# Performance work log

Hardware: AMD Instinct MI355X
Metric: run time of the kernel (lower is better)

The kernel has to match this reference:

```python
import jax, jax.numpy as jnp
import numpy as np

NUM_USER = 100000
NUM_ITEM = 50000
N = NUM_USER + NUM_ITEM          # total nodes
D = 64                            # dim_latent
E = 2400000                       # nnz of sparse graph
NUM_LAYER = 3


def setup_inputs() -> dict:
    key = jax.random.key(0)
    k1, k2, k3, k4, k5 = jax.random.split(key, 5)
    user_emb = jax.random.normal(k1, (NUM_USER, D), dtype=jnp.float32)
    item_emb = jax.random.normal(k2, (NUM_ITEM, D), dtype=jnp.float32)
    graph_rows = jax.random.randint(k3, (E,), 0, N, dtype=jnp.int32)
    graph_cols = jax.random.randint(k4, (E,), 0, N, dtype=jnp.int32)
    # normalized-adjacency-like small positive values
    graph_vals = jax.random.uniform(k5, (E,), dtype=jnp.float32) * 0.01
    return {
        "user_emb": user_emb,
        "item_emb": item_emb,
        "graph_vals": graph_vals,
        "graph_rows": graph_rows,
        "graph_cols": graph_cols,
    }


def _spmm(vals, rows, cols, x):
    # sparse [N,N] @ dense [N,D] via gather + segment_sum
    gathered = vals[:, None] * x[cols]            # [E, D]
    return jax.ops.segment_sum(gathered, rows, num_segments=N)  # [N, D]


def reference(user_emb, item_emb, graph_vals, graph_rows, graph_cols):
    all_emb = jnp.concatenate([user_emb, item_emb], axis=0)   # [N, D]
    acc = all_emb
    emb = all_emb
    for _ in range(NUM_LAYER):
        emb = _spmm(graph_vals, graph_rows, graph_cols, emb)
        acc = acc + emb
    light_out = acc / jnp.float32(NUM_LAYER + 1)              # mean over layer dim
    return (light_out, user_emb, item_emb)
```

## Files before the change

kernel.cpp:

```cpp
#include <hip/hip_runtime.h>


#define NUM_USER 100000
#define NUM_ITEM 50000
#define NTOT     150000
#define DIM      64
#define NEDGE    2400000
#define ND       (NTOT * DIM)

#define RPB    256
#define NB     586
#define CAP    4736
#define CHUNK  4096
#define NCHUNK 586
#define EPT    16

static __device__ __forceinline__ unsigned short f2bf(float f) {
    unsigned u = __float_as_uint(f);
    u += 0x7FFFu + ((u >> 16) & 1u);
    return (unsigned short)(u >> 16);
}
static __device__ __forceinline__ float bf2f(unsigned short h) {
    return __uint_as_float(((unsigned)h) << 16);
}

__global__ __launch_bounds__(256) void initcur_kernel(int* __restrict__ cursor) {
    const int i = blockIdx.x * blockDim.x + threadIdx.x;
    if (i < NB) cursor[i] = i * CAP;
}

__global__ __launch_bounds__(256) void phaseA_kernel(
    const int*   __restrict__ rows,
    const int*   __restrict__ cols,
    const float* __restrict__ vals,
    int*            __restrict__ cursor,
    unsigned*       __restrict__ crG,
    unsigned short* __restrict__ vbG)
{
    __shared__ unsigned       s_cr[CHUNK];
    __shared__ unsigned short s_vb[CHUNK];
    __shared__ unsigned short s_bk[CHUNK];
    __shared__ int s_hist[NB];
    __shared__ int s_scan[NB];
    __shared__ int s_dst[NB];
    __shared__ int s_cur[NB];
    __shared__ int s_part[256];

    const int t    = threadIdx.x;
    const int base = blockIdx.x * CHUNK;
    const int n    = min(CHUNK, NEDGE - base);

    for (int i = t; i < NB; i += 256) s_hist[i] = 0;
    __syncthreads();

    int            mrow[EPT];
    unsigned       mcol[EPT];
    unsigned short mvb[EPT];
#pragma unroll
    for (int k = 0; k < EPT; ++k) {
        const int i = t + k * 256;
        if (i < n) {
            const int e = base + i;
            mrow[k] = rows[e];
            mcol[k] = (unsigned)cols[e];
            mvb[k]  = f2bf(vals[e]);
            atomicAdd(&s_hist[mrow[k] >> 8], 1);
        } else mrow[k] = -1;
    }
    __syncthreads();

    int loc[3]; int ssum = 0;
#pragma unroll
    for (int k = 0; k < 3; ++k) {
        const int i = t * 3 + k;
        loc[k] = (i < NB) ? s_hist[i] : 0;
        ssum += loc[k];
    }
    s_part[t] = ssum;
    __syncthreads();
    for (int o = 1; o < 256; o <<= 1) {
        const int v = (t >= o) ? s_part[t - o] : 0;
        __syncthreads();
        s_part[t] += v;
        __syncthreads();
    }
    int run = s_part[t] - ssum;
#pragma unroll
    for (int k = 0; k < 3; ++k) {
        const int i = t * 3 + k;
        if (i < NB) { s_scan[i] = run; run += loc[k]; }
    }
    __syncthreads();

    for (int i = t; i < NB; i += 256) {
        const int c = s_hist[i];
        s_dst[i] = c ? atomicAdd(&cursor[i], c) : 0;
        s_cur[i] = s_scan[i];
    }
    __syncthreads();

#pragma unroll
    for (int k = 0; k < EPT; ++k) {
        if (mrow[k] >= 0) {
            const int b   = mrow[k] >> 8;
            const int pos = atomicAdd(&s_cur[b], 1);
            s_cr[pos] = mcol[k] | ((unsigned)(mrow[k] & 255) << 18);
            s_vb[pos] = mvb[k];
            s_bk[pos] = (unsigned short)b;
        }
    }
    __syncthreads();

    for (int p = t; p < n; p += 256) {
        const int b = s_bk[p];
        const int g = s_dst[b] + (p - s_scan[b]);
        crG[g] = s_cr[p];
        vbG[g] = s_vb[p];
    }
}

__global__ __launch_bounds__(256) void phaseB_kernel(
    const int*      __restrict__ cursor,
    unsigned*       __restrict__ crG,
    unsigned short* __restrict__ vbG,
    int*            __restrict__ rowbeg,
    int*            __restrict__ rowend)
{
    __shared__ unsigned       s_cr[CAP];
    __shared__ unsigned short s_vb[CAP];
    __shared__ unsigned short s_idx[CAP];
    __shared__ int s_hist[RPB];
    __shared__ int s_scan[RPB];
    __shared__ int s_cur[RPB];

    const int b = blockIdx.x, t = threadIdx.x;
    const int gbase = b * CAP;
    const int cnt = cursor[b] - gbase;

    s_hist[t] = 0;
    __syncthreads();
    for (int p = t; p < cnt; p += 256) {
        const unsigned cr = crG[gbase + p];
        s_cr[p] = cr;
        s_vb[p] = vbG[gbase + p];
        atomicAdd(&s_hist[cr >> 18], 1);
    }
    __syncthreads();

    const int h = s_hist[t];
    s_scan[t] = h;
    __syncthreads();
    for (int o = 1; o < 256; o <<= 1) {
        const int v = (t >= o) ? s_scan[t - o] : 0;
        __syncthreads();
        s_scan[t] += v;
        __syncthreads();
    }
    const int excl = s_scan[t] - h;
    s_cur[t] = excl;
    __syncthreads();

    for (int p = t; p < cnt; p += 256) {
        const int r   = s_cr[p] >> 18;
        const int pos = atomicAdd(&s_cur[r], 1);
        s_idx[pos] = (unsigned short)p;
    }
    __syncthreads();

    for (int p = t; p < cnt; p += 256) {
        const int i = s_idx[p];
        crG[gbase + p] = s_cr[i];
        vbG[gbase + p] = s_vb[i];
    }
    const int row = b * RPB + t;
    if (row < NTOT) {
        rowbeg[row] = gbase + excl;
        rowend[row] = gbase + excl + h;
    }
}

__global__ __launch_bounds__(256) void convert_kernel(
    const float* __restrict__ user,
    const float* __restrict__ item,
    unsigned short* __restrict__ xb)
{
    const int nvec  = ND / 4;
    const int userv = NUM_USER * DIM / 4;
    for (int i = blockIdx.x * blockDim.x + threadIdx.x; i < nvec;
         i += gridDim.x * blockDim.x) {
        const float4 v = (i < userv) ? ((const float4*)user)[i]
                                     : ((const float4*)item)[i - userv];
        ushort4 o;
        o.x = f2bf(v.x); o.y = f2bf(v.y); o.z = f2bf(v.z); o.w = f2bf(v.w);
        ((ushort4*)xb)[i] = o;
    }
}

template<int MODE>
__global__ __launch_bounds__(256) void spmm_pull(
    const int*            __restrict__ rowbeg,
    const int*            __restrict__ rowend,
    const unsigned*       __restrict__ crG,
    const unsigned short* __restrict__ vbG,
    const unsigned short* __restrict__ xb,
    unsigned short*       __restrict__ destb,
    float*                __restrict__ acc,
    const float*          __restrict__ user,
    const float*          __restrict__ item,
    float*                __restrict__ out)
{
    const int r    = (blockIdx.x * 256 + threadIdx.x) >> 6;
    const int lane = threadIdx.x & 63;
    const int g    = lane >> 4;
    const int l    = lane & 15;

    const int beg = __builtin_amdgcn_readfirstlane(rowbeg[r]);
    const int end = __builtin_amdgcn_readfirstlane(rowend[r]);

    float r0 = 0.f, r1 = 0.f, r2 = 0.f, r3 = 0.f;
    for (int k = beg + g; k < end; k += 8) {
        const bool h1 = (k + 4) < end;
        const int  k1 = h1 ? k + 4 : k;
        const unsigned c0 = crG[k]  & 0x3FFFFu;
        const unsigned c1 = crG[k1] & 0x3FFFFu;
        const float    v0 = bf2f(vbG[k]);
        const float    v1 = h1 ? bf2f(vbG[k1]) : 0.f;
        const uint2 xa = *reinterpret_cast<const uint2*>(
                             xb + ((size_t)c0 << 6) + (l << 2));
        const uint2 xc = *reinterpret_cast<const uint2*>(
                             xb + ((size_t)c1 << 6) + (l << 2));
        r0 += v0 * bf2f((unsigned short)(xa.x & 0xFFFFu))
            + v1 * bf2f((unsigned short)(xc.x & 0xFFFFu));
        r1 += v0 * bf2f((unsigned short)(xa.x >> 16))
            + v1 * bf2f((unsigned short)(xc.x >> 16));
        r2 += v0 * bf2f((unsigned short)(xa.y & 0xFFFFu))
            + v1 * bf2f((unsigned short)(xc.y & 0xFFFFu));
        r3 += v0 * bf2f((unsigned short)(xa.y >> 16))
            + v1 * bf2f((unsigned short)(xc.y >> 16));
    }
    r0 += __shfl_xor(r0, 16); r0 += __shfl_xor(r0, 32);
    r1 += __shfl_xor(r1, 16); r1 += __shfl_xor(r1, 32);
    r2 += __shfl_xor(r2, 16); r2 += __shfl_xor(r2, 32);
    r3 += __shfl_xor(r3, 16); r3 += __shfl_xor(r3, 32);

    if (g == 0) {
        const int o = r * DIM + (l << 2);
        if (MODE == 0) {
            *reinterpret_cast<float4*>(acc + o) = make_float4(r0, r1, r2, r3);
        } else if (MODE == 1) {
            float4 a = *reinterpret_cast<float4*>(acc + o);
            a.x += r0; a.y += r1; a.z += r2; a.w += r3;
            *reinterpret_cast<float4*>(acc + o) = a;
        } else {
            const float* aep = (r < NUM_USER)
                ? user + (size_t)r * DIM
                : item + (size_t)(r - NUM_USER) * DIM;
            const float4 ae = *reinterpret_cast<const float4*>(aep + (l << 2));
            float4 a = *reinterpret_cast<const float4*>(acc + o);
            float4 lo;
            lo.x = (a.x + r0 + ae.x) * 0.25f;
            lo.y = (a.y + r1 + ae.y) * 0.25f;
            lo.z = (a.z + r2 + ae.z) * 0.25f;
            lo.w = (a.w + r3 + ae.w) * 0.25f;
            *reinterpret_cast<float4*>(out + o)      = lo;
            *reinterpret_cast<float4*>(out + ND + o) = ae;
        }
        if (MODE == 0 || MODE == 1) {
            ushort4 pk;
            pk.x = f2bf(r0); pk.y = f2bf(r1); pk.z = f2bf(r2); pk.w = f2bf(r3);
            *reinterpret_cast<ushort4*>(destb + o) = pk;
        }
    }
}


__global__ __launch_bounds__(256) void spmm_atomic(
    const float* __restrict__ vals, const int* __restrict__ rows,
    const int* __restrict__ cols, const float* __restrict__ x0,
    const float* __restrict__ x1, int split, float* __restrict__ out)
{
    const int lane = threadIdx.x & 63;
    const long wave   = ((long)blockIdx.x * blockDim.x + threadIdx.x) >> 6;
    const long nwaves = ((long)gridDim.x * blockDim.x) >> 6;
    for (long e = wave; e < NEDGE; e += nwaves) {
        const int   r = rows[e];
        const int   c = cols[e];
        const float v = vals[e];
        const float xv = (c < split) ? x0[(long)c * DIM + lane]
                                     : x1[(long)(c - split) * DIM + lane];
        atomicAdd(&out[(long)r * DIM + lane], v * xv);
    }
}

__global__ __launch_bounds__(256) void add2_kernel(
    const float* __restrict__ a, const float* __restrict__ b,
    float* __restrict__ acc)
{
    const int nvec = ND / 4;
    for (int i = blockIdx.x * blockDim.x + threadIdx.x; i < nvec;
         i += gridDim.x * blockDim.x) {
        const float4 av = ((const float4*)a)[i];
        const float4 bv = ((const float4*)b)[i];
        float4 o;
        o.x = av.x + bv.x; o.y = av.y + bv.y;
        o.z = av.z + bv.z; o.w = av.w + bv.w;
        ((float4*)acc)[i] = o;
    }
}

__global__ __launch_bounds__(256) void finalize3_kernel(
    const float* __restrict__ user, const float* __restrict__ item,
    float* __restrict__ out)
{
    const int nvec  = ND / 4;
    const int userv = NUM_USER * DIM / 4;
    for (int i = blockIdx.x * blockDim.x + threadIdx.x; i < nvec;
         i += gridDim.x * blockDim.x) {
        const float4 ae = (i < userv) ? ((const float4*)user)[i]
                                      : ((const float4*)item)[i - userv];
        const float4 ac = ((const float4*)out)[i];
        const float4 e3 = ((const float4*)(out + ND))[i];
        float4 lo;
        lo.x = (ae.x + ac.x + e3.x) * 0.25f;
        lo.y = (ae.y + ac.y + e3.y) * 0.25f;
        lo.z = (ae.z + ac.z + e3.z) * 0.25f;
        lo.w = (ae.w + ac.w + e3.w) * 0.25f;
        ((float4*)out)[i] = lo;
        ((float4*)(out + ND))[i] = ae;
    }
}


extern "C" void kernel_launch(void* const* d_in, const int* in_sizes, int n_in,
                              void* d_out, int out_size, void* d_ws, size_t ws_size,
                              hipStream_t stream) {
    const float* user = (const float*)d_in[0];
    const float* item = (const float*)d_in[1];
    const float* vals = (const float*)d_in[2];
    const int*   rows = (const int*)d_in[3];
    const int*   cols = (const int*)d_in[4];

    float* out = (float*)d_out;
    float* acc = out;

    char* w = (char*)d_ws;
    unsigned short* xb0 = (unsigned short*)w;
    unsigned short* xb1 = xb0 + ND;
    unsigned*       crG = (unsigned*)(xb1 + ND);
    int*   rowbeg = (int*)(crG + (size_t)NB * CAP);
    int*   rowend = rowbeg + NTOT;
    int*   cursor = rowend + NTOT;
    unsigned short* vbG = (unsigned short*)(cursor + NB);
    const size_t ws_need = (size_t)ND * 4 + (size_t)NB * CAP * 6
                         + (size_t)(2 * NTOT + NB) * 4 + 64;

    if (ws_size >= ws_need) {
        initcur_kernel<<<(NB + 255) / 256, 256, 0, stream>>>(cursor);
        phaseA_kernel<<<NCHUNK, 256, 0, stream>>>(rows, cols, vals, cursor, crG, vbG);
        phaseB_kernel<<<NB, 256, 0, stream>>>(cursor, crG, vbG, rowbeg, rowend);
        convert_kernel<<<2048, 256, 0, stream>>>(user, item, xb0);

        const int spmm_blocks = NTOT / 4;
        spmm_pull<0><<<spmm_blocks, 256, 0, stream>>>(rowbeg, rowend, crG, vbG,
            xb0, xb1, acc, nullptr, nullptr, nullptr);
        spmm_pull<1><<<spmm_blocks, 256, 0, stream>>>(rowbeg, rowend, crG, vbG,
            xb1, xb0, acc, nullptr, nullptr, nullptr);
        spmm_pull<2><<<spmm_blocks, 256, 0, stream>>>(rowbeg, rowend, crG, vbG,
            xb0, nullptr, acc, user, item, out);
    } else {
        float* bufA = (float*)d_ws;
        float* out1 = out + ND;
        const size_t nd_bytes = (size_t)ND * sizeof(float);
        hipMemsetAsync(out1, 0, nd_bytes, stream);
        spmm_atomic<<<2048, 256, 0, stream>>>(vals, rows, cols, user, item, NUM_USER, out1);
        hipMemsetAsync(bufA, 0, nd_bytes, stream);
        spmm_atomic<<<2048, 256, 0, stream>>>(vals, rows, cols, out1, out1, NTOT, bufA);
        add2_kernel<<<2048, 256, 0, stream>>>(out1, bufA, acc);
        hipMemsetAsync(out1, 0, nd_bytes, stream);
        spmm_atomic<<<2048, 256, 0, stream>>>(vals, rows, cols, bufA, bufA, NTOT, out1);
        finalize3_kernel<<<2048, 256, 0, stream>>>(user, item, out);
    }
}
```

Before: 268.4 us.

## Store propagated embeddings in FP8 and fuse conversion into bucketing kernel

Switches the intermediate embedding buffers from bf16 to FP8 (e4m3), using hardware pack and unpack conversion builtins. This halves the bytes fetched per gathered neighbor row in each SpMM layer. The input conversion now runs in extra blocks of the phaseA bucketing kernel rather than a separate launch, and the cursor init kernel becomes a memset with offsets added in phaseA. The gather loop is unrolled to four edges per group, using packed float2 accumulation. FP8's much lower mantissa precision risks accuracy loss across three layers.

```diff
diff --git a/kernel.cpp b/kernel.cpp
--- a/kernel.cpp
+++ b/kernel.cpp
@@ -14,6 +14,9 @@
 #define CHUNK  4096
 #define NCHUNK 586
 #define EPT    16
+#define CVTB   1024
+
+typedef float v2f __attribute__((ext_vector_type(2)));
 
 static __device__ __forceinline__ unsigned short f2bf(float f) {
     unsigned u = __float_as_uint(f);
@@ -23,10 +26,11 @@
 static __device__ __forceinline__ float bf2f(unsigned short h) {
     return __uint_as_float(((unsigned)h) << 16);
 }
-
-__global__ __launch_bounds__(256) void initcur_kernel(int* __restrict__ cursor) {
-    const int i = blockIdx.x * blockDim.x + threadIdx.x;
-    if (i < NB) cursor[i] = i * CAP;
+static __device__ __forceinline__ unsigned pk_fp8x4(float a, float b, float c, float d) {
+    int p = 0;
+    p = __builtin_amdgcn_cvt_pk_fp8_f32(a, b, p, false);
+    p = __builtin_amdgcn_cvt_pk_fp8_f32(c, d, p, true);
+    return (unsigned)p;
 }
 
 __global__ __launch_bounds__(256) void phaseA_kernel(
@@ -35,7 +39,10 @@
     const float* __restrict__ vals,
     int*            __restrict__ cursor,
     unsigned*       __restrict__ crG,
-    unsigned short* __restrict__ vbG)
+    unsigned short* __restrict__ vbG,
+    const float*    __restrict__ user,
+    const float*    __restrict__ item,
+    unsigned*       __restrict__ xq)
 {
     __shared__ unsigned       s_cr[CHUNK];
     __shared__ unsigned short s_vb[CHUNK];
@@ -45,6 +52,18 @@
     __shared__ int s_dst[NB];
     __shared__ int s_cur[NB];
     __shared__ int s_part[256];
+
+    if (blockIdx.x >= NCHUNK) {
+        const int nvec  = ND / 4;
+        const int userv = NUM_USER * DIM / 4;
+        for (int i = (blockIdx.x - NCHUNK) * 256 + threadIdx.x; i < nvec;
+             i += CVTB * 256) {
+            const float4 v = (i < userv) ? ((const float4*)user)[i]
+                                         : ((const float4*)item)[i - userv];
+            xq[i] = pk_fp8x4(v.x, v.y, v.z, v.w);
+        }
+        return;
+    }
 
     const int t    = threadIdx.x;
     const int base = blockIdx.x * CHUNK;
@@ -94,7 +113,7 @@
 
     for (int i = t; i < NB; i += 256) {
         const int c = s_hist[i];
-        s_dst[i] = c ? atomicAdd(&cursor[i], c) : 0;
+        s_dst[i] = i * CAP + (c ? atomicAdd(&cursor[i], c) : 0);
         s_cur[i] = s_scan[i];
     }
     __syncthreads();
@@ -135,7 +154,7 @@
 
     const int b = blockIdx.x, t = threadIdx.x;
     const int gbase = b * CAP;
-    const int cnt = cursor[b] - gbase;
+    const int cnt = cursor[b];
 
     s_hist[t] = 0;
     __syncthreads();
@@ -176,23 +195,6 @@
     if (row < NTOT) {
         rowbeg[row] = gbase + excl;
         rowend[row] = gbase + excl + h;
-    }
-}
-
-__global__ __launch_bounds__(256) void convert_kernel(
-    const float* __restrict__ user,
-    const float* __restrict__ item,
-    unsigned short* __restrict__ xb)
-{
-    const int nvec  = ND / 4;
-    const int userv = NUM_USER * DIM / 4;
-    for (int i = blockIdx.x * blockDim.x + threadIdx.x; i < nvec;
-         i += gridDim.x * blockDim.x) {
-        const float4 v = (i < userv) ? ((const float4*)user)[i]
-                                     : ((const float4*)item)[i - userv];
-        ushort4 o;
-        o.x = f2bf(v.x); o.y = f2bf(v.y); o.z = f2bf(v.z); o.w = f2bf(v.w);
-        ((ushort4*)xb)[i] = o;
     }
 }
 
@@ -202,8 +204,8 @@
     const int*            __restrict__ rowend,
     const unsigned*       __restrict__ crG,
     const unsigned short* __restrict__ vbG,
-    const unsigned short* __restrict__ xb,
-    unsigned short*       __restrict__ destb,
+    const unsigned char*  __restrict__ xq,
+    unsigned*             __restrict__ destq,
     float*                __restrict__ acc,
     const float*          __restrict__ user,
     const float*          __restrict__ item,
@@ -217,27 +219,43 @@
     const int beg = __builtin_amdgcn_readfirstlane(rowbeg[r]);
     const int end = __builtin_amdgcn_readfirstlane(rowend[r]);
 
-    float r0 = 0.f, r1 = 0.f, r2 = 0.f, r3 = 0.f;
-    for (int k = beg + g; k < end; k += 8) {
-        const bool h1 = (k + 4) < end;
-        const int  k1 = h1 ? k + 4 : k;
+    v2f a01 = {0.f, 0.f}, a23 = {0.f, 0.f};
+    for (int k = beg + g; k < end; k += 16) {
+        const bool h1 = (k + 4)  < end;
+        const bool h2 = (k + 8)  < end;
+        const bool h3 = (k + 12) < end;
+        const int  k1 = h1 ? k + 4  : k;
+        const int  k2 = h2 ? k + 8  : k;
+        const int  k3 = h3 ? k + 12 : k;
+
         const unsigned c0 = crG[k]  & 0x3FFFFu;
         const unsigned c1 = crG[k1] & 0x3FFFFu;
-        const float    v0 = bf2f(vbG[k]);
-        const float    v1 = h1 ? bf2f(vbG[k1]) : 0.f;
-        const uint2 xa = *reinterpret_cast<const uint2*>(
-                             xb + ((size_t)c0 << 6) + (l << 2));
-        const uint2 xc = *reinterpret_cast<const uint2*>(
-                             xb + ((size_t)c1 << 6) + (l << 2));
-        r0 += v0 * bf2f((unsigned short)(xa.x & 0xFFFFu))
-            + v1 * bf2f((unsigned short)(xc.x & 0xFFFFu));
-        r1 += v0 * bf2f((unsigned short)(xa.x >> 16))
-            + v1 * bf2f((unsigned short)(xc.x >> 16));
-        r2 += v0 * bf2f((unsigned short)(xa.y & 0xFFFFu))
-            + v1 * bf2f((unsigned short)(xc.y & 0xFFFFu));
-        r3 += v0 * bf2f((unsigned short)(xa.y >> 16))
-            + v1 * bf2f((unsigned short)(xc.y >> 16));
-    }
+        const unsigned c2 = crG[k2] & 0x3FFFFu;
+        const unsigned c3 = crG[k3] & 0x3FFFFu;
+        const float v0 = bf2f(vbG[k]);
+        const float v1 = h1 ? bf2f(vbG[k1]) : 0.f;
+        const float v2 = h2 ? bf2f(vbG[k2]) : 0.f;
+        const float v3 = h3 ? bf2f(vbG[k3]) : 0.f;
+
+        const unsigned w0 = *reinterpret_cast<const unsigned*>(
+                                xq + ((size_t)c0 << 6) + (l << 2));
+        const unsigned w1 = *reinterpret_cast<const unsigned*>(
+                                xq + ((size_t)c1 << 6) + (l << 2));
+        const unsigned w2 = *reinterpret_cast<const unsigned*>(
+                                xq + ((size_t)c2 << 6) + (l << 2));
+        const unsigned w3 = *reinterpret_cast<const unsigned*>(
+                                xq + ((size_t)c3 << 6) + (l << 2));
+
+        a01 += (v2f){v0, v0} * __builtin_amdgcn_cvt_pk_f32_fp8((int)w0, false);
+        a23 += (v2f){v0, v0} * __builtin_amdgcn_cvt_pk_f32_fp8((int)w0, true);
+        a01 += (v2f){v1, v1} * __builtin_amdgcn_cvt_pk_f32_fp8((int)w1, false);
+        a23 += (v2f){v1, v1} * __builtin_amdgcn_cvt_pk_f32_fp8((int)w1, true);
+        a01 += (v2f){v2, v2} * __builtin_amdgcn_cvt_pk_f32_fp8((int)w2, false);
+        a23 += (v2f){v2, v2} * __builtin_amdgcn_cvt_pk_f32_fp8((int)w2, true);
+        a01 += (v2f){v3, v3} * __builtin_amdgcn_cvt_pk_f32_fp8((int)w3, false);
+        a23 += (v2f){v3, v3} * __builtin_amdgcn_cvt_pk_f32_fp8((int)w3, true);
+    }
+    float r0 = a01.x, r1 = a01.y, r2 = a23.x, r3 = a23.y;
     r0 += __shfl_xor(r0, 16); r0 += __shfl_xor(r0, 32);
     r1 += __shfl_xor(r1, 16); r1 += __shfl_xor(r1, 32);
     r2 += __shfl_xor(r2, 16); r2 += __shfl_xor(r2, 32);
@@ -266,9 +284,7 @@
             *reinterpret_cast<float4*>(out + ND + o) = ae;
         }
         if (MODE == 0 || MODE == 1) {
-            ushort4 pk;
-            pk.x = f2bf(r0); pk.y = f2bf(r1); pk.z = f2bf(r2); pk.w = f2bf(r3);
-            *reinterpret_cast<ushort4*>(destb + o) = pk;
+            destq[(r * DIM >> 2) + l] = pk_fp8x4(r0, r1, r2, r3);
         }
     }
 }
@@ -344,29 +360,29 @@
     float* acc = out;
 
     char* w = (char*)d_ws;
-    unsigned short* xb0 = (unsigned short*)w;
-    unsigned short* xb1 = xb0 + ND;
-    unsigned*       crG = (unsigned*)(xb1 + ND);
+    unsigned char* xq0 = (unsigned char*)w;
+    unsigned char* xq1 = xq0 + ND;
+    unsigned*      crG = (unsigned*)(xq1 + ND);
     int*   rowbeg = (int*)(crG + (size_t)NB * CAP);
     int*   rowend = rowbeg + NTOT;
     int*   cursor = rowend + NTOT;
     unsigned short* vbG = (unsigned short*)(cursor + NB);
-    const size_t ws_need = (size_t)ND * 4 + (size_t)NB * CAP * 6
+    const size_t ws_need = (size_t)ND * 2 + (size_t)NB * CAP * 6
                          + (size_t)(2 * NTOT + NB) * 4 + 64;
 
     if (ws_size >= ws_need) {
-        initcur_kernel<<<(NB + 255) / 256, 256, 0, stream>>>(cursor);
-        phaseA_kernel<<<NCHUNK, 256, 0, stream>>>(rows, cols, vals, cursor, crG, vbG);
+        hipMemsetAsync(cursor, 0, (size_t)NB * 4, stream);
+        phaseA_kernel<<<NCHUNK + CVTB, 256, 0, stream>>>(
+            rows, cols, vals, cursor, crG, vbG, user, item, (unsigned*)xq0);
         phaseB_kernel<<<NB, 256, 0, stream>>>(cursor, crG, vbG, rowbeg, rowend);
-        convert_kernel<<<2048, 256, 0, stream>>>(user, item, xb0);
 
         const int spmm_blocks = NTOT / 4;
         spmm_pull<0><<<spmm_blocks, 256, 0, stream>>>(rowbeg, rowend, crG, vbG,
-            xb0, xb1, acc, nullptr, nullptr, nullptr);
+            xq0, (unsigned*)xq1, acc, nullptr, nullptr, nullptr);
         spmm_pull<1><<<spmm_blocks, 256, 0, stream>>>(rowbeg, rowend, crG, vbG,
-            xb1, xb0, acc, nullptr, nullptr, nullptr);
+            xq1, (unsigned*)xq0, acc, nullptr, nullptr, nullptr);
         spmm_pull<2><<<spmm_blocks, 256, 0, stream>>>(rowbeg, rowend, crG, vbG,
-            xb0, nullptr, acc, user, item, out);
+            xq0, nullptr, acc, user, item, out);
     } else {
         float* bufA = (float*)d_ws;
         float* out1 = out + ND;
```

After: 253.9 us. 5.4% less time.
